# Performance work log

Measured on AMD Instinct MI355X. Metric: run time of the kernel, lower is better.

The kernel has to match this reference:

```python
import jax, jax.numpy as jnp
import numpy as np

K, D = 512, 256

def setup_inputs() -> dict:
    key = jax.random.key(0)
    k1, k2 = jax.random.split(key)
    z_e = jax.random.normal(k1, (64, D, 32, 32), dtype=jnp.float32)
    # matches nn.Embedding weight init uniform_(-1/K, 1/K)
    codebook = jax.random.uniform(k2, (K, D), dtype=jnp.float32, minval=-1.0 / K, maxval=1.0 / K)
    return {"z_e": z_e, "codebook": codebook}

def reference(z_e, codebook):
    N, Dd, H, W = z_e.shape
    # NCHW -> (N*H*W, D) tokens
    x = jnp.transpose(z_e, (0, 2, 3, 1)).reshape(-1, Dd)
    x_sq = jnp.sum(x * x, axis=1, keepdims=True)            # [T, 1]
    w_sq = jnp.sum(codebook * codebook, axis=1)             # [K]
    dists = x_sq - 2.0 * (x @ codebook.T) + w_sq[None, :]   # [T, K]
    q = jnp.argmin(dists, axis=1)                           # [T]
    z_q = codebook[q]                                       # [T, D] gather
    z_q = z_q.reshape(N, H, W, Dd).transpose(0, 3, 1, 2)    # back to NCHW
    q = q.reshape(N, H, W).astype(jnp.int64)
    return (q, z_q)
```

## Files before the change

### kernel.cpp

```cpp
#include <hip/hip_runtime.h>
#include <float.h>
#include <math.h>


#define KCODES 512
#define DDIM   256
#define HWSZ   1024
#define TTOK   65536
#define TPB    64
#define NBLK   (TTOK / TPB)
#define NCHUNK 16
#define MARGIN 1.0e-3f

#define HW_OFF 33792
#define BK_OFF 35840
#define LDS_SZ 36096
#define ZQ_PITCH 528

typedef short bf16x8 __attribute__((ext_vector_type(8)));
typedef float f32x16 __attribute__((ext_vector_type(16)));
typedef float f32x4  __attribute__((ext_vector_type(4)));

__device__ inline unsigned short bf16rne(float x) {
    union { float f; unsigned u; } a; a.f = x;
    unsigned r = a.u + (0x7fffu + ((a.u >> 16) & 1u));
    return (unsigned short)(r >> 16);
}
__device__ inline float bf16tof(unsigned short h) {
    union { unsigned u; float f; } b; b.u = ((unsigned)h) << 16; return b.f;
}

__device__ __forceinline__ void top4_insert(float m, int c, float fb[4], int fi[4]) {
    #pragma unroll
    for (int l = 0; l < 4; ++l) {
        const bool s = m > fb[l];
        const float nm = s ? fb[l] : m;
        const int   nc = s ? fi[l] : c;
        fb[l] = s ? m : fb[l];
        fi[l] = s ? c : fi[l];
        m = nm; c = nc;
    }
}
__device__ __forceinline__ void top8_insert(float m, int c, float fb[8], int fi[8]) {
    #pragma unroll
    for (int l = 0; l < 8; ++l) {
        const bool s = m > fb[l];
        const float nm = s ? fb[l] : m;
        const int   nc = s ? fi[l] : c;
        fb[l] = s ? m : fb[l];
        fi[l] = s ? c : fi[l];
        m = nm; c = nc;
    }
}

__global__ __launch_bounds__(256) void vq_prep(const float* __restrict__ cb,
                                               unsigned char* __restrict__ wsw,
                                               float* __restrict__ wsq) {
    const int tid = threadIdx.x;
    const int gid = blockIdx.x * 256 + tid;
    {
        const int k = gid >> 5, o = gid & 31;
        const int d0 = o * 8, c = o >> 1, half = o & 1;
        unsigned hi[4], lo[4];
        #pragma unroll
        for (int jj = 0; jj < 4; ++jj) {
            float v0 = cb[k * DDIM + d0 + 2 * jj];
            float v1 = cb[k * DDIM + d0 + 2 * jj + 1];
            unsigned short h0 = bf16rne(v0), h1 = bf16rne(v1);
            unsigned short l0 = bf16rne(v0 - bf16tof(h0));
            unsigned short l1 = bf16rne(v1 - bf16tof(h1));
            hi[jj] = (unsigned)h0 | ((unsigned)h1 << 16);
            lo[jj] = (unsigned)l0 | ((unsigned)l1 << 16);
        }
        const int tile = k >> 5, lane2 = (k & 31) + 32 * half;
        *(uint4*)(wsw + ((size_t)((c * 2 + 0) * 16 + tile) * 1024) + lane2 * 16) = make_uint4(hi[0], hi[1], hi[2], hi[3]);
        *(uint4*)(wsw + ((size_t)((c * 2 + 1) * 16 + tile) * 1024) + lane2 * 16) = make_uint4(lo[0], lo[1], lo[2], lo[3]);
    }
    if (blockIdx.x < 32) {
        const int k = blockIdx.x * 16 + (tid >> 4);
        const int s = tid & 15, h2 = s >> 3, j2 = s & 7;
        const float* p = cb + (size_t)k * DDIM + h2 * 128 + j2;
        float v[16];
        #pragma unroll
        for (int i = 0; i < 16; ++i) v[i] = p[i * 8];
        float rr;
        {
#pragma clang fp contract(off)
            rr = v[0] * v[0];
            #pragma unroll
            for (int i = 1; i < 16; ++i) { float sq = v[i] * v[i]; rr = rr + sq; }
        }
        float t = rr;
        t = t + __shfl_xor(t, 1);
        t = t + __shfl_xor(t, 2);
        t = t + __shfl_xor(t, 4);
        t = t + __shfl_xor(t, 8);
        if (s == 0) wsq[k] = t;
    }
}

__global__ __launch_bounds__(512, 4) void vq_main(const float* __restrict__ z_e,
                                                  const float* __restrict__ cb,
                                                  const float* __restrict__ wsq,
                                                  const unsigned char* __restrict__ wsw,
                                                  float* __restrict__ out) {
    __shared__ __align__(16) unsigned char lds[LDS_SZ];

    const int tid = threadIdx.x;
    const int wv = tid >> 6, lane = tid & 63;
    const int tbase = blockIdx.x * TPB;
    const int n = tbase >> 10, hw0 = tbase & (HWSZ - 1);
    const float* zb = z_e + (size_t)n * (DDIM * HWSZ) + hw0;

    {
        const int tok = tid & 63, g = tid >> 6;
        const int mtS = tok >> 5;
        const int lbase = (tok & 31) * 16;
        #pragma unroll
        for (int o = 0; o < 4; ++o) {
            const int d0 = g * 32 + o * 8;
            float v[8];
            #pragma unroll
            for (int j = 0; j < 8; ++j) v[j] = zb[(size_t)(d0 + j) * HWSZ + tok];
            unsigned hi[4];
            #pragma unroll
            for (int jj = 0; jj < 4; ++jj) {
                unsigned short h0 = bf16rne(v[2 * jj]), h1 = bf16rne(v[2 * jj + 1]);
                hi[jj] = (unsigned)h0 | ((unsigned)h1 << 16);
            }
            const int c = d0 >> 4;
            const int off2 = lbase + 512 * ((d0 >> 3) & 1);
            *(uint4*)(lds + (mtS * 16 + c) * 1024 + off2) = make_uint4(hi[0], hi[1], hi[2], hi[3]);
        }
    }
    ((float*)(lds + HW_OFF))[tid] = 0.5f * wsq[tid];

    __syncthreads();

    const int qc = wv >> 1;
    const int mt = wv & 1;
    const int hh = lane >> 5;
    const float* hwsqL = (const float*)(lds + HW_OFF);

    #define LDW(c, p, t)   (*(const bf16x8*)(wsw + ((size_t)(((c) * 2 + (p)) * 16 + (t)) * 1024) + lane * 16))
    #define LDA(mm, c)     (*(const bf16x8*)(lds + ((mm) * 16 + (c)) * 1024 + lane * 16))

    float fb[4] = {-FLT_MAX, -FLT_MAX, -FLT_MAX, -FLT_MAX};
    int   fi[4] = {KCODES, KCODES, KCODES, KCODES};

    #pragma unroll
    for (int pr = 0; pr < 2; ++pr) {
        const int ct0 = qc * 4 + 2 * pr;
        f32x16 a0, a1;
        #pragma unroll
        for (int r = 0; r < 16; ++r) { a0[r] = 0.f; a1[r] = 0.f; }
        bf16x8 Xc[2], Wc[2][4];
        Xc[0] = LDA(mt, 0);
        Wc[0][0] = LDW(0, 0, ct0); Wc[0][1] = LDW(0, 1, ct0);
        Wc[0][2] = LDW(0, 0, ct0 + 1); Wc[0][3] = LDW(0, 1, ct0 + 1);
        #pragma unroll
        for (int c = 0; c < NCHUNK; ++c) {
            const int cur = c & 1, nxt = cur ^ 1;
            if (c + 1 < NCHUNK) {
                Xc[nxt] = LDA(mt, c + 1);
                Wc[nxt][0] = LDW(c + 1, 0, ct0); Wc[nxt][1] = LDW(c + 1, 1, ct0);
                Wc[nxt][2] = LDW(c + 1, 0, ct0 + 1); Wc[nxt][3] = LDW(c + 1, 1, ct0 + 1);
            }
            a0 = __builtin_amdgcn_mfma_f32_32x32x16_bf16(Wc[cur][0], Xc[cur], a0, 0, 0, 0);
            a1 = __builtin_amdgcn_mfma_f32_32x32x16_bf16(Wc[cur][2], Xc[cur], a1, 0, 0, 0);
            a0 = __builtin_amdgcn_mfma_f32_32x32x16_bf16(Wc[cur][1], Xc[cur], a0, 0, 0, 0);
            a1 = __builtin_amdgcn_mfma_f32_32x32x16_bf16(Wc[cur][3], Xc[cur], a1, 0, 0, 0);
        }
        #pragma unroll
        for (int rq = 0; rq < 4; ++rq) {
            const f32x4 h40 = *(const f32x4*)(hwsqL + ct0 * 32 + rq * 8 + 4 * hh);
            const f32x4 h41 = *(const f32x4*)(hwsqL + (ct0 + 1) * 32 + rq * 8 + 4 * hh);
            #pragma unroll
            for (int rr = 0; rr < 4; ++rr) {
                top4_insert(a0[rq * 4 + rr] - h40[rr], ct0 * 32 + rr + 8 * rq + 4 * hh, fb, fi);
                top4_insert(a1[rq * 4 + rr] - h41[rr], (ct0 + 1) * 32 + rr + 8 * rq + 4 * hh, fb, fi);
            }
        }
    }

    {
        float sb[4]; int si[4];
        #pragma unroll
        for (int c = 0; c < 4; ++c) { sb[c] = __shfl_xor(fb[c], 32); si[c] = __shfl_xor(fi[c], 32); }
        #pragma unroll
        for (int c = 0; c < 4; ++c) top4_insert(sb[c], si[c], fb, fi);
    }

    __syncthreads();
    float* candm = (float*)lds;
    int*   candi = (int*)(lds + 4096);
    int*   wlCnt = (int*)(lds + 8192);
    int*   wlTok = (int*)(lds + 8208);
    int*   wlGi  = (int*)(lds + 8464);
    float* wlG   = (float*)(lds + 10512);
    int*   bkArr = (int*)(lds + BK_OFF);
    if (lane < 32) {
        const int slot = (qc * 64 + mt * 32 + lane) * 4;
        #pragma unroll
        for (int c = 0; c < 4; ++c) { candm[slot + c] = fb[c]; candi[slot + c] = fi[c]; }
    }
    if (tid == 0) *wlCnt = 0;
    __syncthreads();

    if (tid < TPB) {
        float g[8]; int gi[8];
        #pragma unroll
        for (int c = 0; c < 8; ++c) { g[c] = -FLT_MAX; gi[c] = KCODES; }
        #pragma unroll
        for (int q4 = 0; q4 < 4; ++q4) {
            const int slot = (q4 * 64 + tid) * 4;
            #pragma unroll
            for (int c = 0; c < 4; ++c) top8_insert(candm[slot + c], candi[slot + c], g, gi);
        }
        if (g[0] - g[1] > MARGIN) {
            out[tbase + tid] = (float)gi[0];
            bkArr[tid] = gi[0];
        } else {
            const int slot = atomicAdd(wlCnt, 1);
            wlTok[slot] = tid;
            #pragma unroll
            for (int c = 0; c < 8; ++c) { wlGi[slot * 8 + c] = gi[c]; wlG[slot * 8 + c] = g[c]; }
        }
    }
    __syncthreads();

    {
        const int nIt = *wlCnt;
        for (int it = wv; it < nIt; it += 8) {
            const int tok = wlTok[it];
            const float g0 = wlG[it * 8];
            const float* xa = zb + tok;

            float xsq;
            {
                const int h2 = (lane >> 3) & 1, j2 = lane & 7;
                float v[16];
                if (lane < 16) {
                    #pragma unroll
                    for (int i = 0; i < 16; ++i)
                        v[i] = xa[(size_t)(h2 * 128 + i * 8 + j2) * HWSZ];
                } else {
                    #pragma unroll
                    for (int i = 0; i < 16; ++i) v[i] = 0.f;
                }
                float rr;
                {
#pragma clang fp contract(off)
                    rr = v[0] * v[0];
                    #pragma unroll
                    for (int i = 1; i < 16; ++i) { float sq = v[i] * v[i]; rr = rr + sq; }
                }
                float t = rr;
                t = t + __shfl_xor(t, 1);
                t = t + __shfl_xor(t, 2);
                t = t + __shfl_xor(t, 4);
                t = t + __shfl_xor(t, 8);
                xsq = __shfl(t, 0);
            }

            double xv[4];
            #pragma unroll
            for (int i = 0; i < 4; ++i)
                xv[i] = (double)xa[(size_t)(lane + 64 * i) * HWSZ];

            float bestd = FLT_MAX; int bestk = KCODES;
            for (int c = 0; c < 8; ++c) {
                const float gc = wlG[it * 8 + c];
                if (c > 0 && g0 - gc > MARGIN) break;
                const int idx = wlGi[it * 8 + c];
                const float* wr = cb + (size_t)idx * DDIM;
                double A = 0.0;
                #pragma unroll
                for (int i = 0; i < 4; ++i)
                    A = fma((double)wr[lane + 64 * i], xv[i], A);
                A = A + __shfl_xor(A, 1);
                A = A + __shfl_xor(A, 2);
                A = A + __shfl_xor(A, 4);
                A = A + __shfl_xor(A, 8);
                A = A + __shfl_xor(A, 16);
                A = A + __shfl_xor(A, 32);
                float dist;
                {
#pragma clang fp contract(off)
                    const float xw = (float)A;
                    const float t1 = xsq - 2.0f * xw;
                    dist = t1 + wsq[idx];
                }
                if (dist < bestd || (dist == bestd && idx < bestk)) { bestd = dist; bestk = idx; }
            }
            if (lane == 0) {
                out[tbase + tok] = (float)bestk;
                bkArr[tok] = bestk;
            }
        }
    }

    #pragma unroll
    for (int r = 0; r < 2; ++r) {
        __syncthreads();
        {
            #pragma unroll
            for (int rr = 0; rr < 8; ++rr) {
                const int row = wv * 8 + rr;
                const int bk = bkArr[row];
                const float2 vv = *(const float2*)(cb + (size_t)bk * DDIM + r * 128 + lane * 2);
                *(float2*)(lds + row * ZQ_PITCH + lane * 8) = vv;
            }
        }
        __syncthreads();
        {
            const int tk = tid & 63, s = tid >> 6;
            float* zq = out + TTOK + (size_t)n * (DDIM * HWSZ) + hw0 + tk;
            #pragma unroll
            for (int i = 0; i < 16; i += 4) {
                const f32x4 v = *(const f32x4*)(lds + tk * ZQ_PITCH + (s * 16 + i) * 4);
                #pragma unroll
                for (int j = 0; j < 4; ++j)
                    zq[(size_t)(r * 128 + s * 16 + i + j) * HWSZ] = v[j];
            }
        }
    }
}

extern "C" void kernel_launch(void* const* d_in, const int* in_sizes, int n_in,
                              void* d_out, int out_size, void* d_ws, size_t ws_size,
                              hipStream_t stream) {
    const float* z_e = (const float*)d_in[0];
    const float* cb  = (const float*)d_in[1];
    float* out = (float*)d_out;
    float* wsq = (float*)d_ws;
    unsigned char* wsw = (unsigned char*)d_ws + 2048;

    vq_prep<<<64, 256, 0, stream>>>(cb, wsw, wsq);
    vq_main<<<NBLK, 512, 0, stream>>>(z_e, cb, wsq, wsw, out);
}
```

Before: 182.5 us.

## Remap waves so each covers both token tiles over two codebook tiles

Each of the 8 waves now computes both 32-token M tiles against a pair of codebook column tiles, instead of one M tile against four codebook tiles. Each codebook fragment loaded from global memory is reused across two MFMAs, so codebook traffic per wave is halved while X fragments come from LDS. In exchange there are four live accumulators, which raises register pressure, the candidate buffers in LDS double, and the final merge scans 8 candidate groups instead of 4.

Measured after the change: 185.8 us. No clear change (+1.8%).

```diff
diff --git a/kernel.cpp b/kernel.cpp
--- a/kernel.cpp
+++ b/kernel.cpp
@@ -137,39 +137,42 @@
 
     __syncthreads();
 
-    const int qc = wv >> 1;
-    const int mt = wv & 1;
     const int hh = lane >> 5;
+    const int ct0 = wv * 2;
     const float* hwsqL = (const float*)(lds + HW_OFF);
 
     #define LDW(c, p, t)   (*(const bf16x8*)(wsw + ((size_t)(((c) * 2 + (p)) * 16 + (t)) * 1024) + lane * 16))
     #define LDA(mm, c)     (*(const bf16x8*)(lds + ((mm) * 16 + (c)) * 1024 + lane * 16))
 
-    float fb[4] = {-FLT_MAX, -FLT_MAX, -FLT_MAX, -FLT_MAX};
-    int   fi[4] = {KCODES, KCODES, KCODES, KCODES};
-
-    #pragma unroll
-    for (int pr = 0; pr < 2; ++pr) {
-        const int ct0 = qc * 4 + 2 * pr;
-        f32x16 a0, a1;
-        #pragma unroll
-        for (int r = 0; r < 16; ++r) { a0[r] = 0.f; a1[r] = 0.f; }
-        bf16x8 Xc[2], Wc[2][4];
-        Xc[0] = LDA(mt, 0);
-        Wc[0][0] = LDW(0, 0, ct0); Wc[0][1] = LDW(0, 1, ct0);
+    float fbA[4] = {-FLT_MAX, -FLT_MAX, -FLT_MAX, -FLT_MAX};
+    int   fiA[4] = {KCODES, KCODES, KCODES, KCODES};
+    float fbB[4] = {-FLT_MAX, -FLT_MAX, -FLT_MAX, -FLT_MAX};
+    int   fiB[4] = {KCODES, KCODES, KCODES, KCODES};
+
+    {
+        f32x16 a00, a01, a10, a11;
+        #pragma unroll
+        for (int r = 0; r < 16; ++r) { a00[r] = 0.f; a01[r] = 0.f; a10[r] = 0.f; a11[r] = 0.f; }
+        bf16x8 Xc[2][2], Wc[2][4];
+        Xc[0][0] = LDA(0, 0); Xc[0][1] = LDA(1, 0);
+        Wc[0][0] = LDW(0, 0, ct0);     Wc[0][1] = LDW(0, 1, ct0);
         Wc[0][2] = LDW(0, 0, ct0 + 1); Wc[0][3] = LDW(0, 1, ct0 + 1);
         #pragma unroll
         for (int c = 0; c < NCHUNK; ++c) {
             const int cur = c & 1, nxt = cur ^ 1;
             if (c + 1 < NCHUNK) {
-                Xc[nxt] = LDA(mt, c + 1);
-                Wc[nxt][0] = LDW(c + 1, 0, ct0); Wc[nxt][1] = LDW(c + 1, 1, ct0);
+                Wc[nxt][0] = LDW(c + 1, 0, ct0);     Wc[nxt][1] = LDW(c + 1, 1, ct0);
                 Wc[nxt][2] = LDW(c + 1, 0, ct0 + 1); Wc[nxt][3] = LDW(c + 1, 1, ct0 + 1);
-            }
-            a0 = __builtin_amdgcn_mfma_f32_32x32x16_bf16(Wc[cur][0], Xc[cur], a0, 0, 0, 0);
-            a1 = __builtin_amdgcn_mfma_f32_32x32x16_bf16(Wc[cur][2], Xc[cur], a1, 0, 0, 0);
-            a0 = __builtin_amdgcn_mfma_f32_32x32x16_bf16(Wc[cur][1], Xc[cur], a0, 0, 0, 0);
-            a1 = __builtin_amdgcn_mfma_f32_32x32x16_bf16(Wc[cur][3], Xc[cur], a1, 0, 0, 0);
+                Xc[nxt][0] = LDA(0, c + 1); Xc[nxt][1] = LDA(1, c + 1);
+            }
+            a00 = __builtin_amdgcn_mfma_f32_32x32x16_bf16(Wc[cur][0], Xc[cur][0], a00, 0, 0, 0);
+            a10 = __builtin_amdgcn_mfma_f32_32x32x16_bf16(Wc[cur][0], Xc[cur][1], a10, 0, 0, 0);
+            a01 = __builtin_amdgcn_mfma_f32_32x32x16_bf16(Wc[cur][2], Xc[cur][0], a01, 0, 0, 0);
+            a11 = __builtin_amdgcn_mfma_f32_32x32x16_bf16(Wc[cur][2], Xc[cur][1], a11, 0, 0, 0);
+            a00 = __builtin_amdgcn_mfma_f32_32x32x16_bf16(Wc[cur][1], Xc[cur][0], a00, 0, 0, 0);
+            a10 = __builtin_amdgcn_mfma_f32_32x32x16_bf16(Wc[cur][1], Xc[cur][1], a10, 0, 0, 0);
+            a01 = __builtin_amdgcn_mfma_f32_32x32x16_bf16(Wc[cur][3], Xc[cur][0], a01, 0, 0, 0);
+            a11 = __builtin_amdgcn_mfma_f32_32x32x16_bf16(Wc[cur][3], Xc[cur][1], a11, 0, 0, 0);
         }
         #pragma unroll
         for (int rq = 0; rq < 4; ++rq) {
@@ -177,8 +180,12 @@
             const f32x4 h41 = *(const f32x4*)(hwsqL + (ct0 + 1) * 32 + rq * 8 + 4 * hh);
             #pragma unroll
             for (int rr = 0; rr < 4; ++rr) {
-                top4_insert(a0[rq * 4 + rr] - h40[rr], ct0 * 32 + rr + 8 * rq + 4 * hh, fb, fi);
-                top4_insert(a1[rq * 4 + rr] - h41[rr], (ct0 + 1) * 32 + rr + 8 * rq + 4 * hh, fb, fi);
+                const int code0 = ct0 * 32 + rr + 8 * rq + 4 * hh;
+                const int code1 = (ct0 + 1) * 32 + rr + 8 * rq + 4 * hh;
+                top4_insert(a00[rq * 4 + rr] - h40[rr], code0, fbA, fiA);
+                top4_insert(a01[rq * 4 + rr] - h41[rr], code1, fbA, fiA);
+                top4_insert(a10[rq * 4 + rr] - h40[rr], code0, fbB, fiB);
+                top4_insert(a11[rq * 4 + rr] - h41[rr], code1, fbB, fiB);
             }
         }
     }
@@ -186,23 +193,30 @@
     {
         float sb[4]; int si[4];
         #pragma unroll
-        for (int c = 0; c < 4; ++c) { sb[c] = __shfl_xor(fb[c], 32); si[c] = __shfl_xor(fi[c], 32); }
-        #pragma unroll
-        for (int c = 0; c < 4; ++c) top4_insert(sb[c], si[c], fb, fi);
+        for (int c = 0; c < 4; ++c) { sb[c] = __shfl_xor(fbA[c], 32); si[c] = __shfl_xor(fiA[c], 32); }
+        #pragma unroll
+        for (int c = 0; c < 4; ++c) top4_insert(sb[c], si[c], fbA, fiA);
+        #pragma unroll
+        for (int c = 0; c < 4; ++c) { sb[c] = __shfl_xor(fbB[c], 32); si[c] = __shfl_xor(fiB[c], 32); }
+        #pragma unroll
+        for (int c = 0; c < 4; ++c) top4_insert(sb[c], si[c], fbB, fiB);
     }
 
     __syncthreads();
     float* candm = (float*)lds;
-    int*   candi = (int*)(lds + 4096);
-    int*   wlCnt = (int*)(lds + 8192);
-    int*   wlTok = (int*)(lds + 8208);
-    int*   wlGi  = (int*)(lds + 8464);
-    float* wlG   = (float*)(lds + 10512);
+    int*   candi = (int*)(lds + 8192);
+    int*   wlCnt = (int*)(lds + 16384);
+    int*   wlTok = (int*)(lds + 16400);
+    int*   wlGi  = (int*)(lds + 16656);
+    float* wlG   = (float*)(lds + 18704);
     int*   bkArr = (int*)(lds + BK_OFF);
     if (lane < 32) {
-        const int slot = (qc * 64 + mt * 32 + lane) * 4;
-        #pragma unroll
-        for (int c = 0; c < 4; ++c) { candm[slot + c] = fb[c]; candi[slot + c] = fi[c]; }
+        const int slot0 = (wv * 64 + lane) * 4;
+        const int slot1 = (wv * 64 + 32 + lane) * 4;
+        #pragma unroll
+        for (int c = 0; c < 4; ++c) { candm[slot0 + c] = fbA[c]; candi[slot0 + c] = fiA[c]; }
+        #pragma unroll
+        for (int c = 0; c < 4; ++c) { candm[slot1 + c] = fbB[c]; candi[slot1 + c] = fiB[c]; }
     }
     if (tid == 0) *wlCnt = 0;
     __syncthreads();
@@ -212,8 +226,8 @@
         #pragma unroll
         for (int c = 0; c < 8; ++c) { g[c] = -FLT_MAX; gi[c] = KCODES; }
         #pragma unroll
-        for (int q4 = 0; q4 < 4; ++q4) {
-            const int slot = (q4 * 64 + tid) * 4;
+        for (int w8 = 0; w8 < 8; ++w8) {
+            const int slot = (w8 * 64 + tid) * 4;
             #pragma unroll
             for (int c = 0; c < 4; ++c) top8_insert(candm[slot + c], candi[slot + c], g, gi);
         }
```
